# Performance work log

Measured on AMD Instinct MI355X. Metric: run time of the kernel, lower is better.

The kernel has to match this reference:

```python
import jax, jax.numpy as jnp
import numpy as np

N = 50000      # nodes
E = 800000     # edges (avg degree 16)
IN = 128       # in_channels
H = 256        # hidden_channels
EPS = 1e-5     # BatchNorm eps


def setup_inputs() -> dict:
    key = jax.random.key(0)
    ks = iter(jax.random.split(key, 40))
    nrm = lambda shape, s: jax.random.normal(next(ks), shape, dtype=jnp.float32) * s
    d = {}
    d["x"] = nrm((N, IN), 1.0)
    d["edge_index"] = jax.random.randint(next(ks), (2, E), 0, N, dtype=jnp.int32)
    # SAGEConv layers: lin_l (neighbors, with bias) + lin_r (root, no bias); BatchNorm params
    dims = [(IN, H), (H, H), (H, H)]
    for i, (fi, fo) in enumerate(dims):
        s = 1.0 / np.sqrt(fi)
        d[f"w_l{i}"] = nrm((fo, fi), s)
        d[f"b_l{i}"] = nrm((fo,), s)
        d[f"w_r{i}"] = nrm((fo, fi), s)
        d[f"g{i}"] = jnp.ones((fo,), jnp.float32)
        d[f"be{i}"] = nrm((fo,), 0.1)
        d[f"rm{i}"] = nrm((fo,), 0.1)
        d[f"rv{i}"] = jax.random.uniform(next(ks), (fo,), jnp.float32, 0.5, 1.5)
    # predictor MLP: H->H, H->H//2, H//2->1
    for j, (fi, fo) in enumerate([(H, H), (H, H // 2), (H // 2, 1)], start=1):
        s = 1.0 / np.sqrt(fi)
        d[f"pw{j}"] = nrm((fo, fi), s)
        d[f"pb{j}"] = nrm((fo,), s)
    return d


def _sage(x, src, dst, w_l, b_l, w_r):
    # mean aggregation of neighbor messages (gather by src, scatter-add by dst)
    msum = jax.ops.segment_sum(x[src], dst, num_segments=N)       # [N, F]
    cnt = jax.ops.segment_sum(jnp.ones((src.shape[0], 1), x.dtype), dst, num_segments=N)
    mean = msum / jnp.maximum(cnt, 1.0)
    return mean @ w_l.T + b_l + x @ w_r.T


def _bn(x, g, be, rm, rv):
    return (x - rm) * jax.lax.rsqrt(rv + EPS) * g + be


def reference(x, edge_index,
              w_l0, b_l0, w_r0, g0, be0, rm0, rv0,
              w_l1, b_l1, w_r1, g1, be1, rm1, rv1,
              w_l2, b_l2, w_r2, g2, be2, rm2, rv2,
              pw1, pb1, pw2, pb2, pw3, pb3):
    src, dst = edge_index[0], edge_index[1]
    layers = [
        (w_l0, b_l0, w_r0, g0, be0, rm0, rv0),
        (w_l1, b_l1, w_r1, g1, be1, rm1, rv1),
        (w_l2, b_l2, w_r2, g2, be2, rm2, rv2),
    ]
    for (wl, bl, wr, g, be, rm, rv) in layers:
        x = _sage(x, src, dst, wl, bl, wr)
        x = jax.nn.relu(_bn(x, g, be, rm, rv))
        # dropout: identity in eval mode
    h = jax.nn.relu(x @ pw1.T + pb1)
    h = jax.nn.relu(h @ pw2.T + pb2)
    return jax.nn.sigmoid(h @ pw3.T + pb3)   # [N, 1]
```

## Files before the change

### kernel.cpp

```cpp
#include <hip/hip_runtime.h>
#include <hip/hip_fp16.h>

#define NNODES 50000
#define NEDGES 800000

typedef _Float16 f16;
typedef f16 f16x8 __attribute__((ext_vector_type(8)));
typedef f16 f16x4 __attribute__((ext_vector_type(4)));
typedef float f32x4 __attribute__((ext_vector_type(4)));

#define GLOAD_LDS16(g, l) __builtin_amdgcn_global_load_lds( \
    (const __attribute__((address_space(1))) void*)(g), \
    (__attribute__((address_space(3))) void*)(l), 16, 0, 0)


__global__ void k_deg(const int* __restrict__ dst, int* __restrict__ deg, int E) {
    int i = blockIdx.x * blockDim.x + threadIdx.x;
    int stride = gridDim.x * blockDim.x;
    for (; i < E; i += stride) atomicAdd(&deg[dst[i]], 1);
}

__global__ void k_bsum(const int* __restrict__ deg, int* __restrict__ bsum, int n) {
    __shared__ int s[256];
    int i = blockIdx.x * 256 + threadIdx.x;
    s[threadIdx.x] = (i < n) ? ((deg[i] + 7) & ~7) : 0;
    __syncthreads();
    for (int off = 128; off; off >>= 1) {
        if (threadIdx.x < off) s[threadIdx.x] += s[threadIdx.x + off];
        __syncthreads();
    }
    if (threadIdx.x == 0) bsum[blockIdx.x] = s[0];
}

__global__ void k_scan_bsum(int* __restrict__ bsum, int nb) {
    int lane = threadIdx.x & 63;
    int carry = 0;
    for (int base = 0; base < nb; base += 64) {
        int i = base + lane;
        int v = (i < nb) ? bsum[i] : 0;
        int orig = v;
        for (int off = 1; off < 64; off <<= 1) {
            int x = __shfl_up(v, off);
            if (lane >= off) v += x;
        }
        if (i < nb) bsum[i] = carry + v - orig;
        carry += __shfl(v, 63);
    }
}

__global__ void k_offsets(const int* __restrict__ deg, const int* __restrict__ bsum,
                          int* __restrict__ offs, int n) {
    __shared__ int s[256];
    int t = threadIdx.x;
    int i = blockIdx.x * 256 + t;
    int v = (i < n) ? ((deg[i] + 7) & ~7) : 0;
    s[t] = v;
    __syncthreads();
    for (int off = 1; off < 256; off <<= 1) {
        int x = (t >= off) ? s[t - off] : 0;
        __syncthreads();
        s[t] += x;
        __syncthreads();
    }
    if (i < n) offs[i] = bsum[blockIdx.x] + s[t] - v;
    if (i == n - 1) offs[n] = bsum[blockIdx.x] + s[t];
}

__global__ void k_scatter(const int* __restrict__ src, const int* __restrict__ dst,
                          const int* __restrict__ offs, int* __restrict__ cursor,
                          int* __restrict__ csr, int E) {
    int i = blockIdx.x * blockDim.x + threadIdx.x;
    int stride = gridDim.x * blockDim.x;
    for (; i < E; i += stride) {
        int d = dst[i];
        int p = atomicAdd(&cursor[d], 1);
        csr[offs[d] + p] = src[i];
    }
}

__global__ void k_pad(const int* __restrict__ deg, const int* __restrict__ offs,
                      int* __restrict__ csr, int n) {
    int i = blockIdx.x * blockDim.x + threadIdx.x;
    if (i >= n) return;
    int d = deg[i], pd = (d + 7) & ~7;
    int base = offs[i];
    for (int p = d; p < pd; ++p) csr[base + p] = NNODES;
}


__global__ void k_prep(const float* __restrict__ x, f16* __restrict__ h0, int n4,
                       const float* __restrict__ pw3, f16* __restrict__ pw3f) {
    int gid = blockIdx.x * blockDim.x + threadIdx.x;
    int gstride = gridDim.x * blockDim.x;
    for (int i = gid; i < n4; i += gstride) {
        float4 v = ((const float4*)x)[i];
        f16x4 o;
        o[0] = (f16)v.x; o[1] = (f16)v.y; o[2] = (f16)v.z; o[3] = (f16)v.w;
        ((f16x4*)h0)[i] = o;
    }
    if (gid < 32) {
        float4 v = ((const float4*)pw3)[gid];
        f16x4 o;
        o[0] = (f16)v.x; o[1] = (f16)v.y; o[2] = (f16)v.z; o[3] = (f16)v.w;
        ((f16x4*)pw3f)[gid] = o;
    }
}


#define NPK 8
struct PackSeg { const float* w; f16* p; int FO; int K; };
struct PackArgs { PackSeg s[NPK]; };

__global__ void k_packw(PackArgs a) {
    int gid = blockIdx.x * blockDim.x + threadIdx.x;
    int gstride = gridDim.x * blockDim.x;
    for (int sgi = 0; sgi < NPK; ++sgi) {
        PackSeg sg = a.s[sgi];
        int total = sg.FO * sg.K / 8;
        int KS = sg.K >> 5;
        for (int t = gid; t < total; t += gstride) {
            int lane = t & 63;
            int tile = t >> 6;
            int ks = tile % KS, nt = tile / KS;
            int row = nt * 16 + (lane & 15);
            int col = ks * 32 + (lane >> 4) * 8;
            const float4* src = (const float4*)(sg.w + (size_t)row * sg.K + col);
            float4 v0 = src[0], v1 = src[1];
            f16x8 o;
            o[0] = (f16)v0.x; o[1] = (f16)v0.y; o[2] = (f16)v0.z; o[3] = (f16)v0.w;
            o[4] = (f16)v1.x; o[5] = (f16)v1.y; o[6] = (f16)v1.z; o[7] = (f16)v1.w;
            ((f16x8*)sg.p)[t] = o;
        }
    }
}


struct AffSeg { const float *b, *g, *be, *rm, *rv; float *cs, *cb; int n; int isbn; };
struct AffArgs { AffSeg s[5]; };

__global__ void k_affine_all(AffArgs a) {
    AffSeg sg = a.s[blockIdx.x];
    int t = threadIdx.x;
    if (t < sg.n) {
        if (sg.isbn) {
            float sc = sg.g[t] * rsqrtf(sg.rv[t] + 1e-5f);
            sg.cs[t] = sc;
            sg.cb[t] = (sg.b[t] - sg.rm[t]) * sc + sg.be[t];
        } else {
            sg.cs[t] = 1.0f;
            sg.cb[t] = sg.b[t];
        }
    }
}

template <int F>
__global__ __launch_bounds__(256) void k_aggregate(
    const f16* __restrict__ h, const int* __restrict__ poffs,
    const int* __restrict__ deg, const int* __restrict__ csr,
    f16* __restrict__ mean) {
    constexpr int LPN = F / 8;
    constexpr int NPW = 64 / LPN;
    int tid = threadIdx.x;
    int wave = tid >> 6, lane = tid & 63;
    int node = blockIdx.x * (4 * NPW) + wave * NPW + lane / LPN;
    int t = lane % LPN;
    int beg = poffs[node], end = poffs[node + 1];
    int nb = (end - beg) >> 3;
    const f16x8* hb = (const f16x8*)h;
    float acc[8] = {0.f, 0.f, 0.f, 0.f, 0.f, 0.f, 0.f, 0.f};

    int j = beg;
    for (int p = 0; p + 2 <= nb; p += 2, j += 16) {
        int iA[8], iB[8];
#pragma unroll
        for (int u = 0; u < 8; ++u) iA[u] = csr[j + u];
#pragma unroll
        for (int u = 0; u < 8; ++u) iB[u] = csr[j + 8 + u];
        f16x8 vA[8], vB[8];
#pragma unroll
        for (int u = 0; u < 8; ++u) vA[u] = hb[(size_t)iA[u] * LPN + t];
#pragma unroll
        for (int u = 0; u < 8; ++u) vB[u] = hb[(size_t)iB[u] * LPN + t];
#pragma unroll
        for (int u = 0; u < 8; ++u)
#pragma unroll
            for (int e = 0; e < 8; ++e) acc[e] += (float)vA[u][e];
#pragma unroll
        for (int u = 0; u < 8; ++u)
#pragma unroll
            for (int e = 0; e < 8; ++e) acc[e] += (float)vB[u][e];
    }
    if (nb & 1) {
        int iA[8];
#pragma unroll
        for (int u = 0; u < 8; ++u) iA[u] = csr[j + u];
        f16x8 vA[8];
#pragma unroll
        for (int u = 0; u < 8; ++u) vA[u] = hb[(size_t)iA[u] * LPN + t];
#pragma unroll
        for (int u = 0; u < 8; ++u)
#pragma unroll
            for (int e = 0; e < 8; ++e) acc[e] += (float)vA[u][e];
    }

    int d = deg[node];
    float inv = (d > 0) ? 1.0f / (float)d : 0.0f;
    f16x8 o;
#pragma unroll
    for (int e = 0; e < 8; ++e) o[e] = (f16)(acc[e] * inv);
    ((f16x8*)mean)[(size_t)node * LPN + t] = o;
}

template <int FO, bool FUSE>
__global__ __launch_bounds__(FO * 2, 4) void k_gemm(
    const f16* __restrict__ A1, const f16* __restrict__ A2,
    const f16* __restrict__ W1p, const f16* __restrict__ W2p,
    const float* __restrict__ cs, const float* __restrict__ cb,
    f16* __restrict__ out, const f16* __restrict__ w3,
    const float* __restrict__ pb3, float* __restrict__ outF,
    int M, int K) {
    constexpr int WC = FO / 64;
    constexpr int NT = FO * 2;
    __shared__ f16 As[128 * 64];
    __shared__ float smF[WC][128];
    int tid = threadIdx.x;
    int lane = tid & 63;
    int wave = tid >> 6;
    int wr = wave / WC, wc = wave % WC;
    int m0 = blockIdx.x * 128;
    int lrow = lane & 15;
    int kof8 = (lane >> 4) * 8;
    int KC1 = K >> 6;
    int KS = K >> 5;
    int NC = A2 ? KC1 * 2 : KC1;

    auto stage = [&](int c) {
        int ph = (c >= KC1) ? 1 : 0;
        const char* Ab = (const char*)(ph ? A2 : A1);
        int kb0 = ((c - ph * KC1) << 6) * 2;
        char* Al = (char*)&As[0];
#pragma unroll
        for (int u0 = 0; u0 < 1024; u0 += NT) {
            int u = u0 + tid;
            int row = u >> 3;
            int kb = (u & 7) * 16;
            int grow = m0 + row; if (grow > M - 1) grow = M - 1;
            GLOAD_LDS16(Ab + (size_t)grow * (K * 2) + kb0 + (kb ^ ((row & 7) << 4)), Al + u * 16);
        }
    };

    f32x4 acc[4][4] = {};

    for (int c = 0; c < NC; ++c) {
        stage(c);
        int ph = (c >= KC1) ? 1 : 0;
        const f16x8* Wp = (const f16x8*)(ph ? W2p : W1p);
        int cl = c - ph * KC1;
        f16x8 b[2][4];
#pragma unroll
        for (int kk = 0; kk < 2; ++kk) {
            int ks = cl * 2 + kk;
#pragma unroll
            for (int ni = 0; ni < 4; ++ni) {
                int nt = wc * 4 + ni;
                b[kk][ni] = Wp[((size_t)nt * KS + ks) * 64 + lane];
            }
        }
        __syncthreads();
        const char* Al = (const char*)&As[0];
#pragma unroll
        for (int kk = 0; kk < 2; ++kk) {
            int kb = kof8 * 2 + kk * 64;
            f16x8 a[4];
#pragma unroll
            for (int mi = 0; mi < 4; ++mi) {
                int r = wr * 64 + mi * 16 + lrow;
                a[mi] = *(const f16x8*)(Al + r * 128 + (kb ^ ((r & 7) << 4)));
            }
#pragma unroll
            for (int mi = 0; mi < 4; ++mi)
#pragma unroll
                for (int ni = 0; ni < 4; ++ni)
                    acc[mi][ni] = __builtin_amdgcn_mfma_f32_16x16x32_f16(a[mi], b[kk][ni], acc[mi][ni], 0, 0, 0);
        }
        __syncthreads();
    }

    if constexpr (!FUSE) {
        int rquad = (lane >> 4) * 4;
#pragma unroll
        for (int mi = 0; mi < 4; ++mi) {
#pragma unroll
            for (int ni = 0; ni < 4; ++ni) {
                int col = wc * 64 + ni * 16 + (lane & 15);
                float s = cs[col], cc = cb[col];
#pragma unroll
                for (int r = 0; r < 4; ++r) {
                    int row = m0 + wr * 64 + mi * 16 + rquad + r;
                    if (row < M) {
                        float v = acc[mi][ni][r] * s + cc;
                        v = fmaxf(v, 0.f);
                        out[(size_t)row * FO + col] = (f16)v;
                    }
                }
            }
        }
    } else {
        float b3 = pb3[0];
        float rsum[4][4] = {};
#pragma unroll
        for (int ni = 0; ni < 4; ++ni) {
            int col = wc * 64 + ni * 16 + (lane & 15);
            float w3v = (float)w3[col];
            float cbv = cb[col];
#pragma unroll
            for (int mi = 0; mi < 4; ++mi)
#pragma unroll
                for (int r = 0; r < 4; ++r)
                    rsum[mi][r] += fmaxf(acc[mi][ni][r] + cbv, 0.f) * w3v;
        }
#pragma unroll
        for (int mi = 0; mi < 4; ++mi)
#pragma unroll
            for (int r = 0; r < 4; ++r) {
                float s = rsum[mi][r];
                s += __shfl_xor(s, 1); s += __shfl_xor(s, 2);
                s += __shfl_xor(s, 4); s += __shfl_xor(s, 8);
                if ((lane & 15) == 0)
                    smF[wc][wr * 64 + mi * 16 + (lane >> 4) * 4 + r] = s;
            }
        __syncthreads();
        if (tid < 128) {
            int row = m0 + tid;
            if (row < M) {
                float s = b3;
#pragma unroll
                for (int w = 0; w < WC; ++w) s += smF[w][tid];
                outF[row] = 1.0f / (1.0f + expf(-s));
            }
        }
    }
}


extern "C" void kernel_launch(void* const* d_in, const int* in_sizes, int n_in,
                              void* d_out, int out_size, void* d_ws, size_t ws_size,
                              hipStream_t stream) {
    const float* x = (const float*)d_in[0];
    const int* ei = (const int*)d_in[1];
    const int* src = ei;
    const int* dst = ei + NEDGES;
    const float* w_l[3] = {(const float*)d_in[2], (const float*)d_in[9], (const float*)d_in[16]};
    const float* b_l[3] = {(const float*)d_in[3], (const float*)d_in[10], (const float*)d_in[17]};
    const float* w_r[3] = {(const float*)d_in[4], (const float*)d_in[11], (const float*)d_in[18]};
    const float* g[3]  = {(const float*)d_in[5], (const float*)d_in[12], (const float*)d_in[19]};
    const float* be[3] = {(const float*)d_in[6], (const float*)d_in[13], (const float*)d_in[20]};
    const float* rm[3] = {(const float*)d_in[7], (const float*)d_in[14], (const float*)d_in[21]};
    const float* rv[3] = {(const float*)d_in[8], (const float*)d_in[15], (const float*)d_in[22]};
    const float* pw1 = (const float*)d_in[23]; const float* pb1 = (const float*)d_in[24];
    const float* pw2 = (const float*)d_in[25]; const float* pb2 = (const float*)d_in[26];
    const float* pw3 = (const float*)d_in[27]; const float* pb3 = (const float*)d_in[28];

    char* wsb = (char*)d_ws;
    size_t o = 0;
    auto alloc = [&](size_t b) { size_t r = o; o = (o + b + 255) & ~(size_t)255; return r; };

    int* deg    = (int*)(wsb + alloc(NNODES * 4));
    int* cursor = (int*)(wsb + alloc(NNODES * 4));
    int* poffs  = (int*)(wsb + alloc((NNODES + 1) * 4));
    int* bsum   = (int*)(wsb + alloc(256 * 4));
    int* csr    = (int*)(wsb + alloc((NEDGES + 8 * NNODES) * 4));
    f16* h0   = (f16*)(wsb + alloc((size_t)(NNODES + 1) * 128 * 2));
    f16* hA   = (f16*)(wsb + alloc((size_t)(NNODES + 1) * 256 * 2));
    f16* hB   = (f16*)(wsb + alloc((size_t)(NNODES + 1) * 256 * 2));
    f16* mean = (f16*)(wsb + alloc((size_t)NNODES * 256 * 2));
    f16* wl0p = (f16*)(wsb + alloc(256 * 128 * 2));
    f16* wr0p = (f16*)(wsb + alloc(256 * 128 * 2));
    f16* wl1p = (f16*)(wsb + alloc(256 * 256 * 2));
    f16* wr1p = (f16*)(wsb + alloc(256 * 256 * 2));
    f16* wl2p = (f16*)(wsb + alloc(256 * 256 * 2));
    f16* wr2p = (f16*)(wsb + alloc(256 * 256 * 2));
    f16* pw1p = (f16*)(wsb + alloc(256 * 256 * 2));
    f16* pw2p = (f16*)(wsb + alloc(128 * 256 * 2));
    f16* pw3f = (f16*)(wsb + alloc(128 * 2));
    float* csv[5]; float* cbv[5];
    for (int i = 0; i < 5; ++i) {
        csv[i] = (float*)(wsb + alloc(256 * 4));
        cbv[i] = (float*)(wsb + alloc(256 * 4));
    }

    hipMemsetAsync(deg, 0, NNODES * 4, stream);
    hipMemsetAsync(cursor, 0, NNODES * 4, stream);
    hipMemsetAsync(h0 + (size_t)NNODES * 128, 0, 128 * 2, stream);
    hipMemsetAsync(hA + (size_t)NNODES * 256, 0, 256 * 2, stream);
    hipMemsetAsync(hB + (size_t)NNODES * 256, 0, 256 * 2, stream);
    k_deg<<<3125, 256, 0, stream>>>(dst, deg, NEDGES);
    int nb = (NNODES + 255) / 256;
    k_bsum<<<nb, 256, 0, stream>>>(deg, bsum, NNODES);
    k_scan_bsum<<<1, 64, 0, stream>>>(bsum, nb);
    k_offsets<<<nb, 256, 0, stream>>>(deg, bsum, poffs, NNODES);
    k_scatter<<<3125, 256, 0, stream>>>(src, dst, poffs, cursor, csr, NEDGES);
    k_pad<<<nb, 256, 0, stream>>>(deg, poffs, csr, NNODES);

    k_prep<<<1600, 256, 0, stream>>>(x, h0, NNODES * 128 / 4, pw3, pw3f);
    PackArgs pa;
    pa.s[0] = {w_l[0], wl0p, 256, 128};
    pa.s[1] = {w_r[0], wr0p, 256, 128};
    pa.s[2] = {w_l[1], wl1p, 256, 256};
    pa.s[3] = {w_r[1], wr1p, 256, 256};
    pa.s[4] = {w_l[2], wl2p, 256, 256};
    pa.s[5] = {w_r[2], wr2p, 256, 256};
    pa.s[6] = {pw1,    pw1p, 256, 256};
    pa.s[7] = {pw2,    pw2p, 128, 256};
    k_packw<<<64, 256, 0, stream>>>(pa);

    AffArgs aa;
    for (int i = 0; i < 3; ++i)
        aa.s[i] = {b_l[i], g[i], be[i], rm[i], rv[i], csv[i], cbv[i], 256, 1};
    aa.s[3] = {pb1, nullptr, nullptr, nullptr, nullptr, csv[3], cbv[3], 256, 0};
    aa.s[4] = {pb2, nullptr, nullptr, nullptr, nullptr, csv[4], cbv[4], 128, 0};
    k_affine_all<<<5, 256, 0, stream>>>(aa);

    int gm = (NNODES + 127) / 128;

    k_aggregate<128><<<3125, 256, 0, stream>>>(h0, poffs, deg, csr, mean);
    k_gemm<256, false><<<gm, 512, 0, stream>>>(mean, h0, wl0p, wr0p, csv[0], cbv[0], hA,
                                               nullptr, nullptr, nullptr, NNODES, 128);
    k_aggregate<256><<<6250, 256, 0, stream>>>(hA, poffs, deg, csr, mean);
    k_gemm<256, false><<<gm, 512, 0, stream>>>(mean, hA, wl1p, wr1p, csv[1], cbv[1], hB,
                                               nullptr, nullptr, nullptr, NNODES, 256);
    k_aggregate<256><<<6250, 256, 0, stream>>>(hB, poffs, deg, csr, mean);
    k_gemm<256, false><<<gm, 512, 0, stream>>>(mean, hB, wl2p, wr2p, csv[2], cbv[2], hA,
                                               nullptr, nullptr, nullptr, NNODES, 256);
    k_gemm<256, false><<<gm, 512, 0, stream>>>(hA, nullptr, pw1p, nullptr, csv[3], cbv[3], hB,
                                               nullptr, nullptr, nullptr, NNODES, 256);
    k_gemm<128, true><<<gm, 256, 0, stream>>>(hB, nullptr, pw2p, nullptr, csv[4], cbv[4], nullptr,
                                              pw3f, pb3, (float*)d_out, NNODES, 256);
}
```

Before: 350.8 us.

## Fuse neighbor mean aggregation into SAGE layer GEMM via LDS staging

Replaces the separate aggregate kernel plus GEMM per SAGE layer with one kernel. Each 64-row block gathers neighbor means straight into a swizzled LDS tile, multiplies it by W_l with MFMA, then streams root features through double-buffered LDS for W_r, and applies the BN affine and ReLU. This removes the global write and re-read of the mean tensor and two launches per layer. In exchange, tiles are smaller (64 rows), LDS use per block is large, and gather latency is no longer overlapped with GEMM work from other kernels.

Result: slower. 390.4 us (+11.3%).

```diff
diff --git a/kernel.cpp b/kernel.cpp
--- a/kernel.cpp
+++ b/kernel.cpp
@@ -153,62 +153,172 @@
     }
 }
 
-template <int F>
-__global__ __launch_bounds__(256) void k_aggregate(
+template <int K>
+__global__ __launch_bounds__(256, 3) void k_layer(
     const f16* __restrict__ h, const int* __restrict__ poffs,
     const int* __restrict__ deg, const int* __restrict__ csr,
-    f16* __restrict__ mean) {
-    constexpr int LPN = F / 8;
+    const f16* __restrict__ Wlp, const f16* __restrict__ Wrp,
+    const float* __restrict__ cs, const float* __restrict__ cb,
+    f16* __restrict__ out, int M) {
+    constexpr int KB = K * 2;
+    constexpr int KC1 = K / 64;
+    constexpr int KS = K / 32;
+    constexpr int LPN = K / 8;
     constexpr int NPW = 64 / LPN;
+    __shared__ f16 Am[64 * K];
+    __shared__ f16 Ax[2][64 * 64];
     int tid = threadIdx.x;
-    int wave = tid >> 6, lane = tid & 63;
-    int node = blockIdx.x * (4 * NPW) + wave * NPW + lane / LPN;
-    int t = lane % LPN;
-    int beg = poffs[node], end = poffs[node + 1];
-    int nb = (end - beg) >> 3;
-    const f16x8* hb = (const f16x8*)h;
-    float acc[8] = {0.f, 0.f, 0.f, 0.f, 0.f, 0.f, 0.f, 0.f};
-
-    int j = beg;
-    for (int p = 0; p + 2 <= nb; p += 2, j += 16) {
-        int iA[8], iB[8];
-#pragma unroll
-        for (int u = 0; u < 8; ++u) iA[u] = csr[j + u];
-#pragma unroll
-        for (int u = 0; u < 8; ++u) iB[u] = csr[j + 8 + u];
-        f16x8 vA[8], vB[8];
-#pragma unroll
-        for (int u = 0; u < 8; ++u) vA[u] = hb[(size_t)iA[u] * LPN + t];
-#pragma unroll
-        for (int u = 0; u < 8; ++u) vB[u] = hb[(size_t)iB[u] * LPN + t];
-#pragma unroll
-        for (int u = 0; u < 8; ++u)
-#pragma unroll
-            for (int e = 0; e < 8; ++e) acc[e] += (float)vA[u][e];
-#pragma unroll
-        for (int u = 0; u < 8; ++u)
-#pragma unroll
-            for (int e = 0; e < 8; ++e) acc[e] += (float)vB[u][e];
-    }
-    if (nb & 1) {
-        int iA[8];
-#pragma unroll
-        for (int u = 0; u < 8; ++u) iA[u] = csr[j + u];
-        f16x8 vA[8];
-#pragma unroll
-        for (int u = 0; u < 8; ++u) vA[u] = hb[(size_t)iA[u] * LPN + t];
-#pragma unroll
-        for (int u = 0; u < 8; ++u)
-#pragma unroll
-            for (int e = 0; e < 8; ++e) acc[e] += (float)vA[u][e];
-    }
-
-    int d = deg[node];
-    float inv = (d > 0) ? 1.0f / (float)d : 0.0f;
-    f16x8 o;
-#pragma unroll
-    for (int e = 0; e < 8; ++e) o[e] = (f16)(acc[e] * inv);
-    ((f16x8*)mean)[(size_t)node * LPN + t] = o;
+    int lane = tid & 63, wave = tid >> 6;
+    int m0 = blockIdx.x * 64;
+
+    {
+        int t = lane & (LPN - 1);
+        int sub = lane / LPN;
+        const f16x8* hb = (const f16x8*)h;
+#pragma unroll
+        for (int it = 0; it < 16 / NPW; ++it) {
+            int lr = wave * 16 + it * NPW + sub;
+            int node = m0 + lr;
+            int beg = 0, end = 0, d = 1;
+            if (node < M) { beg = poffs[node]; end = poffs[node + 1]; d = deg[node]; }
+            int nb = (end - beg) >> 3;
+            float acc[8] = {0.f, 0.f, 0.f, 0.f, 0.f, 0.f, 0.f, 0.f};
+            int j = beg;
+            for (int p = 0; p + 2 <= nb; p += 2, j += 16) {
+                int iA[8], iB[8];
+#pragma unroll
+                for (int u = 0; u < 8; ++u) iA[u] = csr[j + u];
+#pragma unroll
+                for (int u = 0; u < 8; ++u) iB[u] = csr[j + 8 + u];
+                f16x8 vA[8], vB[8];
+#pragma unroll
+                for (int u = 0; u < 8; ++u) vA[u] = hb[(size_t)iA[u] * LPN + t];
+#pragma unroll
+                for (int u = 0; u < 8; ++u) vB[u] = hb[(size_t)iB[u] * LPN + t];
+#pragma unroll
+                for (int u = 0; u < 8; ++u)
+#pragma unroll
+                    for (int e = 0; e < 8; ++e) acc[e] += (float)vA[u][e];
+#pragma unroll
+                for (int u = 0; u < 8; ++u)
+#pragma unroll
+                    for (int e = 0; e < 8; ++e) acc[e] += (float)vB[u][e];
+            }
+            if (nb & 1) {
+                int iA[8];
+#pragma unroll
+                for (int u = 0; u < 8; ++u) iA[u] = csr[j + u];
+                f16x8 vA[8];
+#pragma unroll
+                for (int u = 0; u < 8; ++u) vA[u] = hb[(size_t)iA[u] * LPN + t];
+#pragma unroll
+                for (int u = 0; u < 8; ++u)
+#pragma unroll
+                    for (int e = 0; e < 8; ++e) acc[e] += (float)vA[u][e];
+            }
+            float inv = (d > 0) ? 1.0f / (float)d : 0.0f;
+            f16x8 o;
+#pragma unroll
+            for (int e = 0; e < 8; ++e) o[e] = (f16)(acc[e] * inv);
+            *(f16x8*)((char*)Am + lr * KB + ((t * 16) ^ ((lr & 7) << 4))) = o;
+        }
+    }
+
+    auto stageX = [&](int buf, int c) {
+        char* Bl = (char*)&Ax[buf][0];
+        int kb0 = c * 128;
+#pragma unroll
+        for (int u0 = 0; u0 < 512; u0 += 256) {
+            int u = u0 + tid;
+            int row = u >> 3;
+            int kb = (u & 7) * 16;
+            int grow = m0 + row; if (grow > M - 1) grow = M - 1;
+            GLOAD_LDS16((const char*)h + (size_t)grow * KB + kb0 + (kb ^ ((row & 7) << 4)),
+                        Bl + u * 16);
+        }
+    };
+
+    stageX(0, 0);
+    __syncthreads();
+
+    int lrow = lane & 15, kof8 = (lane >> 4) * 8;
+    f32x4 acc[4][4] = {};
+    const f16x8* WpL = (const f16x8*)Wlp;
+    const f16x8* WpR = (const f16x8*)Wrp;
+
+#pragma unroll
+    for (int c = 0; c < KC1; ++c) {
+        f16x8 b[2][4];
+#pragma unroll
+        for (int kk = 0; kk < 2; ++kk) {
+            int ks = c * 2 + kk;
+#pragma unroll
+            for (int ni = 0; ni < 4; ++ni)
+                b[kk][ni] = WpL[((size_t)(wave * 4 + ni) * KS + ks) * 64 + lane];
+        }
+#pragma unroll
+        for (int kk = 0; kk < 2; ++kk) {
+            f16x8 a[4];
+#pragma unroll
+            for (int mi = 0; mi < 4; ++mi) {
+                int r = mi * 16 + lrow;
+                a[mi] = *(const f16x8*)((const char*)Am + r * KB +
+                         ((c * 128 + kk * 64 + kof8 * 2) ^ ((r & 7) << 4)));
+            }
+#pragma unroll
+            for (int mi = 0; mi < 4; ++mi)
+#pragma unroll
+                for (int ni = 0; ni < 4; ++ni)
+                    acc[mi][ni] = __builtin_amdgcn_mfma_f32_16x16x32_f16(a[mi], b[kk][ni], acc[mi][ni], 0, 0, 0);
+        }
+    }
+
+    for (int c = 0; c < KC1; ++c) {
+        if (c) __syncthreads();
+        if (c + 1 < KC1) stageX((c + 1) & 1, c + 1);
+        const char* Bl = (const char*)&Ax[c & 1][0];
+        f16x8 b[2][4];
+#pragma unroll
+        for (int kk = 0; kk < 2; ++kk) {
+            int ks = c * 2 + kk;
+#pragma unroll
+            for (int ni = 0; ni < 4; ++ni)
+                b[kk][ni] = WpR[((size_t)(wave * 4 + ni) * KS + ks) * 64 + lane];
+        }
+#pragma unroll
+        for (int kk = 0; kk < 2; ++kk) {
+            f16x8 a[4];
+#pragma unroll
+            for (int mi = 0; mi < 4; ++mi) {
+                int r = mi * 16 + lrow;
+                a[mi] = *(const f16x8*)(Bl + r * 128 + ((kof8 * 2 + kk * 64) ^ ((r & 7) << 4)));
+            }
+#pragma unroll
+            for (int mi = 0; mi < 4; ++mi)
+#pragma unroll
+                for (int ni = 0; ni < 4; ++ni)
+                    acc[mi][ni] = __builtin_amdgcn_mfma_f32_16x16x32_f16(a[mi], b[kk][ni], acc[mi][ni], 0, 0, 0);
+        }
+    }
+
+    int rquad = (lane >> 4) * 4;
+#pragma unroll
+    for (int mi = 0; mi < 4; ++mi) {
+#pragma unroll
+        for (int ni = 0; ni < 4; ++ni) {
+            int col = wave * 64 + ni * 16 + lrow;
+            float s = cs[col], cc = cb[col];
+#pragma unroll
+            for (int r = 0; r < 4; ++r) {
+                int row = m0 + mi * 16 + rquad + r;
+                if (row < M) {
+                    float v = acc[mi][ni][r] * s + cc;
+                    v = fmaxf(v, 0.f);
+                    out[(size_t)row * 256 + col] = (f16)v;
+                }
+            }
+        }
+    }
 }
 
 template <int FO, bool FUSE>
@@ -373,7 +483,6 @@
     f16* h0   = (f16*)(wsb + alloc((size_t)(NNODES + 1) * 128 * 2));
     f16* hA   = (f16*)(wsb + alloc((size_t)(NNODES + 1) * 256 * 2));
     f16* hB   = (f16*)(wsb + alloc((size_t)(NNODES + 1) * 256 * 2));
-    f16* mean = (f16*)(wsb + alloc((size_t)NNODES * 256 * 2));
     f16* wl0p = (f16*)(wsb + alloc(256 * 128 * 2));
     f16* wr0p = (f16*)(wsb + alloc(256 * 128 * 2));
     f16* wl1p = (f16*)(wsb + alloc(256 * 256 * 2));
@@ -421,17 +530,15 @@
     aa.s[4] = {pb2, nullptr, nullptr, nullptr, nullptr, csv[4], cbv[4], 128, 0};
     k_affine_all<<<5, 256, 0, stream>>>(aa);
 
+    int gl = (NNODES + 63) / 64;
     int gm = (NNODES + 127) / 128;
 
-    k_aggregate<128><<<3125, 256, 0, stream>>>(h0, poffs, deg, csr, mean);
-    k_gemm<256, false><<<gm, 512, 0, stream>>>(mean, h0, wl0p, wr0p, csv[0], cbv[0], hA,
-                                               nullptr, nullptr, nullptr, NNODES, 128);
-    k_aggregate<256><<<6250, 256, 0, stream>>>(hA, poffs, deg, csr, mean);
-    k_gemm<256, false><<<gm, 512, 0, stream>>>(mean, hA, wl1p, wr1p, csv[1], cbv[1], hB,
-                                               nullptr, nullptr, nullptr, NNODES, 256);
-    k_aggregate<256><<<6250, 256, 0, stream>>>(hB, poffs, deg, csr, mean);
-    k_gemm<256, false><<<gm, 512, 0, stream>>>(mean, hB, wl2p, wr2p, csv[2], cbv[2], hA,
-                                               nullptr, nullptr, nullptr, NNODES, 256);
+    k_layer<128><<<gl, 256, 0, stream>>>(h0, poffs, deg, csr, wl0p, wr0p,
+                                         csv[0], cbv[0], hA, NNODES);
+    k_layer<256><<<gl, 256, 0, stream>>>(hA, poffs, deg, csr, wl1p, wr1p,
+                                         csv[1], cbv[1], hB, NNODES);
+    k_layer<256><<<gl, 256, 0, stream>>>(hB, poffs, deg, csr, wl2p, wr2p,
+                                         csv[2], cbv[2], hA, NNODES);
     k_gemm<256, false><<<gm, 512, 0, stream>>>(hA, nullptr, pw1p, nullptr, csv[3], cbv[3], hB,
                                                nullptr, nullptr, nullptr, NNODES, 256);
     k_gemm<128, true><<<gm, 256, 0, stream>>>(hB, nullptr, pw2p, nullptr, csv[4], cbv[4], nullptr,
```

## Double-buffer GEMM LDS staging and fold pad and memset work into kernels

Applied to the files above, without the earlier changes.

The GEMM now stages the next 64-wide K chunk of A into a second LDS buffer while MFMAs run on the current one. This is meant to hide global-to-LDS load latency and drops one barrier per iteration. The CSR padding pass is merged into the scatter kernel, and the zeroing of the sentinel rows moves into the prep kernel. The two deg/cursor memsets become a single contiguous memset, cutting launch count. The cost is double the A-tile LDS per block, which may limit occupancy.

New measurement: 347.0 us. About the same (-1.1%).

```diff
diff --git a/kernel.cpp b/kernel.cpp
--- a/kernel.cpp
+++ b/kernel.cpp
@@ -66,43 +66,49 @@
     if (i == n - 1) offs[n] = bsum[blockIdx.x] + s[t];
 }
 
-__global__ void k_scatter(const int* __restrict__ src, const int* __restrict__ dst,
-                          const int* __restrict__ offs, int* __restrict__ cursor,
-                          int* __restrict__ csr, int E) {
+__global__ void k_scatter_pad(const int* __restrict__ src, const int* __restrict__ dst,
+                              const int* __restrict__ offs, const int* __restrict__ deg,
+                              int* __restrict__ cursor, int* __restrict__ csr,
+                              int E, int n) {
     int i = blockIdx.x * blockDim.x + threadIdx.x;
     int stride = gridDim.x * blockDim.x;
-    for (; i < E; i += stride) {
-        int d = dst[i];
+    for (int e = i; e < E; e += stride) {
+        int d = dst[e];
         int p = atomicAdd(&cursor[d], 1);
-        csr[offs[d] + p] = src[i];
-    }
-}
-
-__global__ void k_pad(const int* __restrict__ deg, const int* __restrict__ offs,
-                      int* __restrict__ csr, int n) {
-    int i = blockIdx.x * blockDim.x + threadIdx.x;
-    if (i >= n) return;
-    int d = deg[i], pd = (d + 7) & ~7;
-    int base = offs[i];
-    for (int p = d; p < pd; ++p) csr[base + p] = NNODES;
+        csr[offs[d] + p] = src[e];
+    }
+    for (int v = i; v < n; v += stride) {
+        int d = deg[v], pd = (d + 7) & ~7;
+        int base = offs[v];
+        for (int p = d; p < pd; ++p) csr[base + p] = NNODES;
+    }
 }
 
 
 __global__ void k_prep(const float* __restrict__ x, f16* __restrict__ h0, int n4,
-                       const float* __restrict__ pw3, f16* __restrict__ pw3f) {
-    int gid = blockIdx.x * blockDim.x + threadIdx.x;
+                       const float* __restrict__ pw3, f16* __restrict__ pw3f,
+                       f16* __restrict__ hA, f16* __restrict__ hB) {
+    int gid0 = blockIdx.x * blockDim.x + threadIdx.x;
     int gstride = gridDim.x * blockDim.x;
-    for (int i = gid; i < n4; i += gstride) {
+    for (int i = gid0; i < n4; i += gstride) {
         float4 v = ((const float4*)x)[i];
         f16x4 o;
         o[0] = (f16)v.x; o[1] = (f16)v.y; o[2] = (f16)v.z; o[3] = (f16)v.w;
         ((f16x4*)h0)[i] = o;
     }
-    if (gid < 32) {
-        float4 v = ((const float4*)pw3)[gid];
+    f16x4 z = {};
+    if (gid0 < 32) {
+        ((f16x4*)(h0 + (size_t)NNODES * 128))[gid0] = z;
+    } else if (gid0 < 96) {
+        ((f16x4*)(hA + (size_t)NNODES * 256))[gid0 - 32] = z;
+    } else if (gid0 < 160) {
+        ((f16x4*)(hB + (size_t)NNODES * 256))[gid0 - 96] = z;
+    } else if (gid0 < 192) {
+        int i = gid0 - 160;
+        float4 v = ((const float4*)pw3)[i];
         f16x4 o;
         o[0] = (f16)v.x; o[1] = (f16)v.y; o[2] = (f16)v.z; o[3] = (f16)v.w;
-        ((f16x4*)pw3f)[gid] = o;
+        ((f16x4*)pw3f)[i] = o;
     }
 }
 
@@ -221,7 +227,7 @@
     int M, int K) {
     constexpr int WC = FO / 64;
     constexpr int NT = FO * 2;
-    __shared__ f16 As[128 * 64];
+    __shared__ f16 As[2][128 * 64];
     __shared__ float smF[WC][128];
     int tid = threadIdx.x;
     int lane = tid & 63;
@@ -234,11 +240,11 @@
     int KS = K >> 5;
     int NC = A2 ? KC1 * 2 : KC1;
 
-    auto stage = [&](int c) {
+    auto stage = [&](int buf, int c) {
         int ph = (c >= KC1) ? 1 : 0;
         const char* Ab = (const char*)(ph ? A2 : A1);
         int kb0 = ((c - ph * KC1) << 6) * 2;
-        char* Al = (char*)&As[0];
+        char* Al = (char*)&As[buf][0];
 #pragma unroll
         for (int u0 = 0; u0 < 1024; u0 += NT) {
             int u = u0 + tid;
@@ -251,8 +257,10 @@
 
     f32x4 acc[4][4] = {};
 
+    stage(0, 0);
+    __syncthreads();
+
     for (int c = 0; c < NC; ++c) {
-        stage(c);
         int ph = (c >= KC1) ? 1 : 0;
         const f16x8* Wp = (const f16x8*)(ph ? W2p : W1p);
         int cl = c - ph * KC1;
@@ -266,8 +274,8 @@
                 b[kk][ni] = Wp[((size_t)nt * KS + ks) * 64 + lane];
             }
         }
-        __syncthreads();
-        const char* Al = (const char*)&As[0];
+        if (c + 1 < NC) stage((c + 1) & 1, c + 1);
+        const char* Al = (const char*)&As[c & 1][0];
 #pragma unroll
         for (int kk = 0; kk < 2; ++kk) {
             int kb = kof8 * 2 + kk * 64;
@@ -365,8 +373,10 @@
     size_t o = 0;
     auto alloc = [&](size_t b) { size_t r = o; o = (o + b + 255) & ~(size_t)255; return r; };
 
-    int* deg    = (int*)(wsb + alloc(NNODES * 4));
-    int* cursor = (int*)(wsb + alloc(NNODES * 4));
+    size_t deg_off = alloc(NNODES * 4);
+    size_t cur_off = alloc(NNODES * 4);
+    int* deg    = (int*)(wsb + deg_off);
+    int* cursor = (int*)(wsb + cur_off);
     int* poffs  = (int*)(wsb + alloc((NNODES + 1) * 4));
     int* bsum   = (int*)(wsb + alloc(256 * 4));
     int* csr    = (int*)(wsb + alloc((NEDGES + 8 * NNODES) * 4));
@@ -389,20 +399,15 @@
         cbv[i] = (float*)(wsb + alloc(256 * 4));
     }
 
-    hipMemsetAsync(deg, 0, NNODES * 4, stream);
-    hipMemsetAsync(cursor, 0, NNODES * 4, stream);
-    hipMemsetAsync(h0 + (size_t)NNODES * 128, 0, 128 * 2, stream);
-    hipMemsetAsync(hA + (size_t)NNODES * 256, 0, 256 * 2, stream);
-    hipMemsetAsync(hB + (size_t)NNODES * 256, 0, 256 * 2, stream);
+    hipMemsetAsync(wsb + deg_off, 0, cur_off - deg_off + NNODES * 4, stream);
     k_deg<<<3125, 256, 0, stream>>>(dst, deg, NEDGES);
     int nb = (NNODES + 255) / 256;
     k_bsum<<<nb, 256, 0, stream>>>(deg, bsum, NNODES);
     k_scan_bsum<<<1, 64, 0, stream>>>(bsum, nb);
     k_offsets<<<nb, 256, 0, stream>>>(deg, bsum, poffs, NNODES);
-    k_scatter<<<3125, 256, 0, stream>>>(src, dst, poffs, cursor, csr, NEDGES);
-    k_pad<<<nb, 256, 0, stream>>>(deg, poffs, csr, NNODES);
-
-    k_prep<<<1600, 256, 0, stream>>>(x, h0, NNODES * 128 / 4, pw3, pw3f);
+    k_scatter_pad<<<3125, 256, 0, stream>>>(src, dst, poffs, deg, cursor, csr, NEDGES, NNODES);
+
+    k_prep<<<1600, 256, 0, stream>>>(x, h0, NNODES * 128 / 4, pw3, pw3f, hA, hB);
     PackArgs pa;
     pa.s[0] = {w_l[0], wl0p, 256, 128};
     pa.s[1] = {w_r[0], wr0p, 256, 128};
```
